# Optimization experiments

Hardware: AMD Instinct MI355X
Metric: run time of the kernel (lower is better)

The kernel has to match this reference:

```python
import jax, jax.numpy as jnp
import numpy as np

D_KEY = 512
D_VALUE = 512
D_MEM_HIDDEN = 64
BATCH = 65536


def setup_inputs() -> dict:
    key = jax.random.key(0)
    ks = jax.random.split(key, 6)
    return {
        "key": jax.random.normal(ks[0], (BATCH, D_KEY), dtype=jnp.float32),
        "value": jax.random.normal(ks[1], (BATCH, D_VALUE), dtype=jnp.float32),
        # memory MLP weights (the stored memory)
        "mem_W1": jax.random.normal(ks[2], (D_MEM_HIDDEN, D_KEY), dtype=jnp.float32) * 0.02,
        "mem_b1": jnp.zeros((D_MEM_HIDDEN,), dtype=jnp.float32),
        "mem_W2": jax.random.normal(ks[3], (D_VALUE, D_MEM_HIDDEN), dtype=jnp.float32) * 0.02,
        "mem_b2": jnp.zeros((D_VALUE,), dtype=jnp.float32),
        # per-dimension precision head
        "prec_W": jax.random.normal(ks[4], (D_VALUE, D_KEY), dtype=jnp.float32) * 0.01,
        "prec_b": jnp.ones((D_VALUE,), dtype=jnp.float32),
    }


def reference(key, value, mem_W1, mem_b1, mem_W2, mem_b2, prec_W, prec_b):
    """Faithful translation of MemoryModule.free_energy.

    F = prec * clamp(value - pred, -3, 3)^2 - log(prec), averaged over d_value.
    """
    # predict: two-layer MLP with exact (erf) GELU, matching torch F.gelu default
    h = jax.nn.gelu(key @ mem_W1.T + mem_b1, approximate=False)  # (B, H)
    pred = h @ mem_W2.T + mem_b2                                  # (B, Dv)
    # precision head: softplus + 0.01, always positive
    prec = jax.nn.softplus(key @ prec_W.T + prec_b) + 0.01        # (B, Dv)
    error = jnp.clip(value - pred, -3.0, 3.0)                     # (B, Dv)
    F_per_dim = prec * error * error - jnp.log(prec)
    F_scalar = F_per_dim.mean(axis=-1)                            # (B,)
    return (F_scalar, pred, prec, error)
```

## Files before the change

### kernel.cpp

```cpp
#include <hip/hip_runtime.h>
#include <hip/hip_bf16.h>

#define BATCH 65536
#define DK 512
#define DV 512
#define DH 64
#define BMR 32

typedef __attribute__((ext_vector_type(8))) short bf16x8;
typedef __attribute__((ext_vector_type(4))) float f32x4;

#define LGKM_BAR() do { asm volatile("s_waitcnt lgkmcnt(0)" ::: "memory"); \
                        __builtin_amdgcn_s_barrier(); } while (0)

__device__ __align__(16) short g_wb[327680];

__device__ __forceinline__ short f2bf(float f) {
    union { __hip_bfloat16 h; short s; } u;
    u.h = __float2bfloat16(f);
    return u.s;
}

__device__ __forceinline__ bf16x8 pack8(float4 a, float4 b) {
    bf16x8 r;
    r[0] = f2bf(a.x); r[1] = f2bf(a.y); r[2] = f2bf(a.z); r[3] = f2bf(a.w);
    r[4] = f2bf(b.x); r[5] = f2bf(b.y); r[6] = f2bf(b.z); r[7] = f2bf(b.w);
    return r;
}

__global__ __launch_bounds__(256) void conv_weights(
    const float* __restrict__ W1, const float* __restrict__ W2,
    const float* __restrict__ Wp)
{
    int f = blockIdx.x * 256 + threadIdx.x;
    int lane = f & 63;
    const float* src; int stride, row, col;
    if (f < 4096) {
        int t = f >> 10, kk = (f >> 6) & 15;
        src = W1; stride = DK;
        row = t * 16 + (lane & 15); col = kk * 32 + (lane >> 4) * 8;
    } else if (f < 8192) {
        int g = f - 4096; int t = g >> 7, kh = (g >> 6) & 1;
        src = W2; stride = DH;
        row = t * 16 + (lane & 15); col = kh * 32 + (lane >> 4) * 8;
    } else {
        int g = f - 8192; int t = g >> 10, kk = (g >> 6) & 15;
        src = Wp; stride = DK;
        row = t * 16 + (lane & 15); col = kk * 32 + (lane >> 4) * 8;
    }
    const float* p = src + (long)row * stride + col;
    float4 a = *reinterpret_cast<const float4*>(p);
    float4 b = *reinterpret_cast<const float4*>(p + 4);
    *reinterpret_cast<bf16x8*>(g_wb + (long)f * 8) = pack8(a, b);
}

#define KOF 0
#define XP  32768
#define XZ  40960

__global__ __launch_bounds__(256, 3) void fused_free_energy(
    const float* __restrict__ key, const float* __restrict__ value,
    const float* __restrict__ b1, const float* __restrict__ b2,
    const float* __restrict__ pb,
    float* __restrict__ outF, float* __restrict__ outPred,
    float* __restrict__ outPrec, float* __restrict__ outErr)
{
    __shared__ __align__(16) char lds[49152];

    const bf16x8* W1F = reinterpret_cast<const bf16x8*>(g_wb);
    const bf16x8* W2F = reinterpret_cast<const bf16x8*>(g_wb + 32768);
    const bf16x8* WpF = reinterpret_cast<const bf16x8*>(g_wb + 65536);

    const int tid  = threadIdx.x;
    const int wave = tid >> 6;
    const int lane = tid & 63;
    const int lh   = lane & 15;
    const int lg   = lane >> 4;
    const long row0 = (long)blockIdx.x * BMR;
    const f32x4 zf = {0.f, 0.f, 0.f, 0.f};

    const int rw = tid >> 4;
    const int cw = (tid & 15) * 4;
    const float* vrow0 = value + (row0 + rw) * (long)DV + cw;
    const float* vrow1 = vrow0 + 16 * (long)DV;

    #pragma unroll
    for (int i = 0; i < 8; ++i) {
        int idx = i * 256 + tid;
        int r = idx >> 6, c8 = idx & 63;
        const float* p = key + (row0 + r) * DK + c8 * 8;
        float4 a = *reinterpret_cast<const float4*>(p);
        float4 b = *reinterpret_cast<const float4*>(p + 4);
        int byte = (r * 1024 + c8 * 16) ^ ((r & 7) << 4);
        *reinterpret_cast<bf16x8*>(lds + KOF + byte) = pack8(a, b);
    }
    LGKM_BAR();

    #define KFRAG(mt, kk) (*reinterpret_cast<const bf16x8*>( \
        lds + KOF + (((mt) * 16384 + lh * 1024 + (kk) * 64 + lg * 16) ^ ((lh & 7) << 4))))

    if (wave < 2) {
        #pragma unroll
        for (int jt = 0; jt < 4; ++jt) {
            f32x4 aE = zf, aO = zf;
            #pragma unroll
            for (int kk = 0; kk < 16; kk += 2) {
                bf16x8 f0 = W1F[(jt * 16 + kk) * 64 + lane];
                bf16x8 f1 = W1F[(jt * 16 + kk + 1) * 64 + lane];
                aE = __builtin_amdgcn_mfma_f32_16x16x32_bf16(f0, KFRAG(wave, kk),     aE, 0, 0, 0);
                aO = __builtin_amdgcn_mfma_f32_16x16x32_bf16(f1, KFRAG(wave, kk + 1), aO, 0, 0, 0);
            }
            float4 b1v = *reinterpret_cast<const float4*>(b1 + jt * 16 + lg * 4);
            float b1a[4] = {b1v.x, b1v.y, b1v.z, b1v.w};
            short hs[4];
            #pragma unroll
            for (int r = 0; r < 4; ++r) {
                float z = aE[r] + aO[r] + b1a[r];
                float g = 0.5f * z * (1.0f + erff(z * 0.70710678f));
                hs[r] = f2bf(g);
            }
            int hb = XP + wave * 2048 + ((lh * 128 + jt * 32 + lg * 8) ^ ((lh & 7) << 4));
            short4 hv = {hs[0], hs[1], hs[2], hs[3]};
            *reinterpret_cast<short4*>(lds + hb) = hv;
        }
    }
    LGKM_BAR();
    bf16x8 hreg[2][2];
    #pragma unroll
    for (int mt = 0; mt < 2; ++mt)
        #pragma unroll
        for (int kh = 0; kh < 2; ++kh) {
            int byte = (lh * 128 + kh * 64 + lg * 16) ^ ((lh & 7) << 4);
            hreg[mt][kh] = *reinterpret_cast<const bf16x8*>(lds + XP + mt * 2048 + byte);
        }
    LGKM_BAR();

    float facc0 = 0.f, facc1 = 0.f;

    #pragma unroll 1
    for (int ph = 0; ph < 8; ++ph) {
        float4 va0 = *reinterpret_cast<const float4*>(vrow0 + ph * 64);
        float4 va1 = *reinterpret_cast<const float4*>(vrow1 + ph * 64);

        const int tt = ph * 4 + wave;
        f32x4 a0 = zf, a1 = zf;
        #pragma unroll
        for (int kk = 0; kk < 16; ++kk) {
            bf16x8 f0 = WpF[(tt * 16 + kk) * 64 + lane];
            a0 = __builtin_amdgcn_mfma_f32_16x16x32_bf16(f0, KFRAG(0, kk), a0, 0, 0, 0);
            a1 = __builtin_amdgcn_mfma_f32_16x16x32_bf16(f0, KFRAG(1, kk), a1, 0, 0, 0);
        }
        f32x4 c0 = zf, c1 = zf;
        #pragma unroll
        for (int kh = 0; kh < 2; ++kh) {
            bf16x8 f = W2F[(tt * 2 + kh) * 64 + lane];
            c0 = __builtin_amdgcn_mfma_f32_16x16x32_bf16(f, hreg[0][kh], c0, 0, 0, 0);
            c1 = __builtin_amdgcn_mfma_f32_16x16x32_bf16(f, hreg[1][kh], c1, 0, 0, 0);
        }

        int nb = tt * 16 + lg * 4;
        float4 b2v = *reinterpret_cast<const float4*>(b2 + nb);
        float4 pbv = *reinterpret_cast<const float4*>(pb + nb);

        {
            f32x4 pz, zz;
            pz[0] = c0[0] + b2v.x; pz[1] = c0[1] + b2v.y;
            pz[2] = c0[2] + b2v.z; pz[3] = c0[3] + b2v.w;
            zz[0] = a0[0] + pbv.x; zz[1] = a0[1] + pbv.y;
            zz[2] = a0[2] + pbv.z; zz[3] = a0[3] + pbv.w;
            int sb = (lh * 256 + wave * 64 + lg * 16) ^ ((lh & 7) << 4);
            *reinterpret_cast<f32x4*>(lds + XP + sb) = pz;
            *reinterpret_cast<f32x4*>(lds + XZ + sb) = zz;
        }
        {
            f32x4 pz, zz;
            pz[0] = c1[0] + b2v.x; pz[1] = c1[1] + b2v.y;
            pz[2] = c1[2] + b2v.z; pz[3] = c1[3] + b2v.w;
            zz[0] = a1[0] + pbv.x; zz[1] = a1[1] + pbv.y;
            zz[2] = a1[2] + pbv.z; zz[3] = a1[3] + pbv.w;
            int row = 16 + lh;
            int sb = (row * 256 + wave * 64 + lg * 16) ^ ((row & 7) << 4);
            *reinterpret_cast<f32x4*>(lds + XP + sb) = pz;
            *reinterpret_cast<f32x4*>(lds + XZ + sb) = zz;
        }
        LGKM_BAR();

        #pragma unroll
        for (int ch = 0; ch < 2; ++ch) {
            int row = rw + ch * 16;
            int rb  = (row * 256 + cw * 4) ^ ((row & 7) << 4);
            float4 pr = *reinterpret_cast<const float4*>(lds + XP + rb);
            float4 zv = *reinterpret_cast<const float4*>(lds + XZ + rb);
            long ga = (row0 + row) * (long)DV + ph * 64 + cw;
            float4 va = (ch == 0) ? va0 : va1;
            float pa[4]  = {pr.x, pr.y, pr.z, pr.w};
            float za[4]  = {zv.x, zv.y, zv.z, zv.w};
            float vaa[4] = {va.x, va.y, va.z, va.w};
            float er[4], pc[4], f = 0.f;
            #pragma unroll
            for (int r = 0; r < 4; ++r) {
                float z = za[r];
                float prec = fmaxf(z, 0.f) + __logf(1.0f + __expf(-fabsf(z))) + 0.01f;
                float e = fminf(fmaxf(vaa[r] - pa[r], -3.f), 3.f);
                pc[r] = prec; er[r] = e;
                f += prec * e * e - __logf(prec);
            }
            float4 pc4 = {pc[0], pc[1], pc[2], pc[3]};
            float4 er4 = {er[0], er[1], er[2], er[3]};
            *reinterpret_cast<float4*>(outPred + ga) = pr;
            *reinterpret_cast<float4*>(outPrec + ga) = pc4;
            *reinterpret_cast<float4*>(outErr  + ga) = er4;
            if (ch == 0) facc0 += f; else facc1 += f;
        }
        LGKM_BAR();
    }

    float* fpart = reinterpret_cast<float*>(lds + XP);
    fpart[rw * 16 + (tid & 15)]        = facc0;
    fpart[(rw + 16) * 16 + (tid & 15)] = facc1;
    __syncthreads();
    if (tid < 32) {
        const float* p = fpart + tid * 16;
        float s = 0.f;
        #pragma unroll
        for (int i = 0; i < 16; ++i) s += p[i];
        outF[row0 + tid] = s * (1.0f / 512.0f);
    }
}

extern "C" void kernel_launch(void* const* d_in, const int* in_sizes, int n_in,
                              void* d_out, int out_size, void* d_ws, size_t ws_size,
                              hipStream_t stream) {
    const float* key   = (const float*)d_in[0];
    const float* value = (const float*)d_in[1];
    const float* W1    = (const float*)d_in[2];
    const float* b1    = (const float*)d_in[3];
    const float* W2    = (const float*)d_in[4];
    const float* b2    = (const float*)d_in[5];
    const float* Wp    = (const float*)d_in[6];
    const float* pb    = (const float*)d_in[7];

    float* outF    = (float*)d_out;
    float* outPred = outF + BATCH;
    float* outPrec = outPred + (long)BATCH * DV;
    float* outErr  = outPrec + (long)BATCH * DV;

    conv_weights<<<160, 256, 0, stream>>>(W1, W2, Wp);
    fused_free_energy<<<BATCH / BMR, 256, 0, stream>>>(key, value, b1, b2, pb,
                                                       outF, outPred, outPrec, outErr);
}
```

Baseline: 249.5 us.

## Double-buffer precision-weight fragments across phases and hoist LDS reads before epilogue

Prefetches the first half of the next phase's precision-head weight fragments into registers (ping-pong buffers pfA/pfB) while the current phase computes, and splits each phase's weight loads so the second half is issued early and overlapped with MFMAs. It also moves the LDS reads of pred/z ahead of a barrier so the global stores and transcendental epilogue no longer sit between two barriers. The cost is higher VGPR pressure from holding 16 extra bf16x8 fragments, which may reduce occupancy.

```diff
diff --git a/kernel.cpp b/kernel.cpp
--- a/kernel.cpp
+++ b/kernel.cpp
@@ -137,82 +137,111 @@
 
     float facc0 = 0.f, facc1 = 0.f;
 
+    bf16x8 pfA[8], pfB[8];
+
+#define LOAD_PF(P, tt) do {                                                       \
+        _Pragma("unroll")                                                         \
+        for (int k = 0; k < 8; ++k) P[k] = WpF[((tt) * 16 + k) * 64 + lane];      \
+    } while (0)
+
+#define PHASE(ph, PC, PN, DO_PREF) do {                                           \
+        const int tt = (ph) * 4 + wave;                                           \
+         \
+        float4 va0 = *reinterpret_cast<const float4*>(vrow0 + (ph) * 64);         \
+        float4 va1 = *reinterpret_cast<const float4*>(vrow1 + (ph) * 64);         \
+         \
+        bf16x8 hi[8];                                                             \
+        _Pragma("unroll")                                                         \
+        for (int k = 0; k < 8; ++k) hi[k] = WpF[(tt * 16 + 8 + k) * 64 + lane];   \
+        f32x4 a0 = zf, a1 = zf, c0 = zf, c1 = zf;                                 \
+        _Pragma("unroll")                                                         \
+        for (int k = 0; k < 8; ++k) {                                             \
+            a0 = __builtin_amdgcn_mfma_f32_16x16x32_bf16(PC[k], KFRAG(0, k), a0, 0, 0, 0); \
+            a1 = __builtin_amdgcn_mfma_f32_16x16x32_bf16(PC[k], KFRAG(1, k), a1, 0, 0, 0); \
+        }                                                                         \
+        _Pragma("unroll")                                                         \
+        for (int kh = 0; kh < 2; ++kh) {                                          \
+            bf16x8 f = W2F[(tt * 2 + kh) * 64 + lane];                            \
+            c0 = __builtin_amdgcn_mfma_f32_16x16x32_bf16(f, hreg[0][kh], c0, 0, 0, 0); \
+            c1 = __builtin_amdgcn_mfma_f32_16x16x32_bf16(f, hreg[1][kh], c1, 0, 0, 0); \
+        }                                                                         \
+        _Pragma("unroll")                                                         \
+        for (int k = 0; k < 8; ++k) {                                             \
+            a0 = __builtin_amdgcn_mfma_f32_16x16x32_bf16(hi[k], KFRAG(0, 8 + k), a0, 0, 0, 0); \
+            a1 = __builtin_amdgcn_mfma_f32_16x16x32_bf16(hi[k], KFRAG(1, 8 + k), a1, 0, 0, 0); \
+        }                                                                         \
+        int nb = tt * 16 + lg * 4;                                                \
+        float4 b2v = *reinterpret_cast<const float4*>(b2 + nb);                   \
+        float4 pbv = *reinterpret_cast<const float4*>(pb + nb);                   \
+        {                                                                         \
+            f32x4 pz, zz;                                                         \
+            pz[0] = c0[0] + b2v.x; pz[1] = c0[1] + b2v.y;                         \
+            pz[2] = c0[2] + b2v.z; pz[3] = c0[3] + b2v.w;                         \
+            zz[0] = a0[0] + pbv.x; zz[1] = a0[1] + pbv.y;                         \
+            zz[2] = a0[2] + pbv.z; zz[3] = a0[3] + pbv.w;                         \
+            int sb = (lh * 256 + wave * 64 + lg * 16) ^ ((lh & 7) << 4);          \
+            *reinterpret_cast<f32x4*>(lds + XP + sb) = pz;                        \
+            *reinterpret_cast<f32x4*>(lds + XZ + sb) = zz;                        \
+        }                                                                         \
+        {                                                                         \
+            f32x4 pz, zz;                                                         \
+            pz[0] = c1[0] + b2v.x; pz[1] = c1[1] + b2v.y;                         \
+            pz[2] = c1[2] + b2v.z; pz[3] = c1[3] + b2v.w;                         \
+            zz[0] = a1[0] + pbv.x; zz[1] = a1[1] + pbv.y;                         \
+            zz[2] = a1[2] + pbv.z; zz[3] = a1[3] + pbv.w;                         \
+            int row = 16 + lh;                                                    \
+            int sb = (row * 256 + wave * 64 + lg * 16) ^ ((row & 7) << 4);        \
+            *reinterpret_cast<f32x4*>(lds + XP + sb) = pz;                        \
+            *reinterpret_cast<f32x4*>(lds + XZ + sb) = zz;                        \
+        }                                                                         \
+                 \
+        if (DO_PREF) LOAD_PF(PN, tt + 4);                                         \
+        LGKM_BAR();                                                               \
+                                      \
+        float4 pr0, zv0, pr1, zv1;                                                \
+        {                                                                         \
+            int rb0 = (rw * 256 + cw * 4) ^ ((rw & 7) << 4);                      \
+            int row1 = rw + 16;                                                   \
+            int rb1 = (row1 * 256 + cw * 4) ^ ((row1 & 7) << 4);                  \
+            pr0 = *reinterpret_cast<const float4*>(lds + XP + rb0);               \
+            zv0 = *reinterpret_cast<const float4*>(lds + XZ + rb0);               \
+            pr1 = *reinterpret_cast<const float4*>(lds + XP + rb1);               \
+            zv1 = *reinterpret_cast<const float4*>(lds + XZ + rb1);               \
+        }                                                                         \
+        LGKM_BAR();                                                               \
+                          \
+        _Pragma("unroll")                                                         \
+        for (int ch = 0; ch < 2; ++ch) {                                          \
+            float4 pr = (ch == 0) ? pr0 : pr1;                                    \
+            float4 zv = (ch == 0) ? zv0 : zv1;                                    \
+            float4 va = (ch == 0) ? va0 : va1;                                    \
+            long ga = (row0 + rw + ch * 16) * (long)DV + (ph) * 64 + cw;          \
+            float pa[4]  = {pr.x, pr.y, pr.z, pr.w};                              \
+            float za[4]  = {zv.x, zv.y, zv.z, zv.w};                              \
+            float vaa[4] = {va.x, va.y, va.z, va.w};                              \
+            float er[4], pc[4], f = 0.f;                                          \
+            _Pragma("unroll")                                                     \
+            for (int r = 0; r < 4; ++r) {                                         \
+                float z = za[r];                                                  \
+                float prec = fmaxf(z, 0.f) + __logf(1.0f + __expf(-fabsf(z))) + 0.01f; \
+                float e = fminf(fmaxf(vaa[r] - pa[r], -3.f), 3.f);                \
+                pc[r] = prec; er[r] = e;                                          \
+                f += prec * e * e - __logf(prec);                                 \
+            }                                                                     \
+            float4 pc4 = {pc[0], pc[1], pc[2], pc[3]};                            \
+            float4 er4 = {er[0], er[1], er[2], er[3]};                            \
+            *reinterpret_cast<float4*>(outPred + ga) = pr;                        \
+            *reinterpret_cast<float4*>(outPrec + ga) = pc4;                       \
+            *reinterpret_cast<float4*>(outErr  + ga) = er4;                       \
+            if (ch == 0) facc0 += f; else facc1 += f;                             \
+        }                                                                         \
+    } while (0)
+
+    LOAD_PF(pfA, wave);
     #pragma unroll 1
-    for (int ph = 0; ph < 8; ++ph) {
-        float4 va0 = *reinterpret_cast<const float4*>(vrow0 + ph * 64);
-        float4 va1 = *reinterpret_cast<const float4*>(vrow1 + ph * 64);
-
-        const int tt = ph * 4 + wave;
-        f32x4 a0 = zf, a1 = zf;
-        #pragma unroll
-        for (int kk = 0; kk < 16; ++kk) {
-            bf16x8 f0 = WpF[(tt * 16 + kk) * 64 + lane];
-            a0 = __builtin_amdgcn_mfma_f32_16x16x32_bf16(f0, KFRAG(0, kk), a0, 0, 0, 0);
-            a1 = __builtin_amdgcn_mfma_f32_16x16x32_bf16(f0, KFRAG(1, kk), a1, 0, 0, 0);
-        }
-        f32x4 c0 = zf, c1 = zf;
-        #pragma unroll
-        for (int kh = 0; kh < 2; ++kh) {
-            bf16x8 f = W2F[(tt * 2 + kh) * 64 + lane];
-            c0 = __builtin_amdgcn_mfma_f32_16x16x32_bf16(f, hreg[0][kh], c0, 0, 0, 0);
-            c1 = __builtin_amdgcn_mfma_f32_16x16x32_bf16(f, hreg[1][kh], c1, 0, 0, 0);
-        }
-
-        int nb = tt * 16 + lg * 4;
-        float4 b2v = *reinterpret_cast<const float4*>(b2 + nb);
-        float4 pbv = *reinterpret_cast<const float4*>(pb + nb);
-
-        {
-            f32x4 pz, zz;
-            pz[0] = c0[0] + b2v.x; pz[1] = c0[1] + b2v.y;
-            pz[2] = c0[2] + b2v.z; pz[3] = c0[3] + b2v.w;
-            zz[0] = a0[0] + pbv.x; zz[1] = a0[1] + pbv.y;
-            zz[2] = a0[2] + pbv.z; zz[3] = a0[3] + pbv.w;
-            int sb = (lh * 256 + wave * 64 + lg * 16) ^ ((lh & 7) << 4);
-            *reinterpret_cast<f32x4*>(lds + XP + sb) = pz;
-            *reinterpret_cast<f32x4*>(lds + XZ + sb) = zz;
-        }
-        {
-            f32x4 pz, zz;
-            pz[0] = c1[0] + b2v.x; pz[1] = c1[1] + b2v.y;
-            pz[2] = c1[2] + b2v.z; pz[3] = c1[3] + b2v.w;
-            zz[0] = a1[0] + pbv.x; zz[1] = a1[1] + pbv.y;
-            zz[2] = a1[2] + pbv.z; zz[3] = a1[3] + pbv.w;
-            int row = 16 + lh;
-            int sb = (row * 256 + wave * 64 + lg * 16) ^ ((row & 7) << 4);
-            *reinterpret_cast<f32x4*>(lds + XP + sb) = pz;
-            *reinterpret_cast<f32x4*>(lds + XZ + sb) = zz;
-        }
-        LGKM_BAR();
-
-        #pragma unroll
-        for (int ch = 0; ch < 2; ++ch) {
-            int row = rw + ch * 16;
-            int rb  = (row * 256 + cw * 4) ^ ((row & 7) << 4);
-            float4 pr = *reinterpret_cast<const float4*>(lds + XP + rb);
-            float4 zv = *reinterpret_cast<const float4*>(lds + XZ + rb);
-            long ga = (row0 + row) * (long)DV + ph * 64 + cw;
-            float4 va = (ch == 0) ? va0 : va1;
-            float pa[4]  = {pr.x, pr.y, pr.z, pr.w};
-            float za[4]  = {zv.x, zv.y, zv.z, zv.w};
-            float vaa[4] = {va.x, va.y, va.z, va.w};
-            float er[4], pc[4], f = 0.f;
-            #pragma unroll
-            for (int r = 0; r < 4; ++r) {
-                float z = za[r];
-                float prec = fmaxf(z, 0.f) + __logf(1.0f + __expf(-fabsf(z))) + 0.01f;
-                float e = fminf(fmaxf(vaa[r] - pa[r], -3.f), 3.f);
-                pc[r] = prec; er[r] = e;
-                f += prec * e * e - __logf(prec);
-            }
-            float4 pc4 = {pc[0], pc[1], pc[2], pc[3]};
-            float4 er4 = {er[0], er[1], er[2], er[3]};
-            *reinterpret_cast<float4*>(outPred + ga) = pr;
-            *reinterpret_cast<float4*>(outPrec + ga) = pc4;
-            *reinterpret_cast<float4*>(outErr  + ga) = er4;
-            if (ch == 0) facc0 += f; else facc1 += f;
-        }
-        LGKM_BAR();
+    for (int pp = 0; pp < 4; ++pp) {
+        PHASE(2 * pp,     pfA, pfB, true);
+        PHASE(2 * pp + 1, pfB, pfA, (pp < 3));
     }
 
     float* fpart = reinterpret_cast<float*>(lds + XP);
```

After: 345.9 us. +38.7%, slower.
